# Optimization experiments

Measured on AMD Instinct MI355X. Metric: run time of the kernel, lower is better.

## Reference

```python
import jax, jax.numpy as jnp
import numpy as np

NUM_HEADS = 8
MASK_NEG = -1e30


def setup_inputs() -> dict:
    key = jax.random.key(0)
    k1, k2, k3 = jax.random.split(key, 3)
    B, S, D = 8, 2048, 128
    queries = jax.random.normal(k1, (B, S, D), dtype=jnp.float32)
    mask = jnp.ones((B, S), dtype=jnp.float32)
    # kernel_size=1 Conv1D with no bias == dense matmul over last dim
    W_q = jax.random.normal(k2, (D, D), dtype=jnp.float32) * (D ** -0.5)
    W_mem = jax.random.normal(k3, (D, 2 * D), dtype=jnp.float32) * (D ** -0.5)
    return {"queries": queries, "mask": mask, "W_q": W_q, "W_mem": W_mem}


def _split_heads(x, h):
    # [B, S, D] -> [B, h, S, D/h]
    B, S, D = x.shape
    return x.reshape(B, S, h, D // h).transpose(0, 2, 1, 3)


def reference(queries, mask, W_q, W_mem):
    B, S, D = queries.shape
    h = NUM_HEADS
    scale = (D // h) ** -0.5
    memory = jnp.einsum('bsd,de->bse', queries, W_mem)   # [B,S,2D]
    query = jnp.einsum('bsd,de->bse', queries, W_q)      # [B,S,D]
    K, V = jnp.split(memory, 2, axis=2)
    Q = _split_heads(query, h) * scale                   # [B,h,S,dh]
    K = _split_heads(K, h)
    V = _split_heads(V, h)
    logits = jnp.einsum('bhqd,bhkd->bhqk', Q, K)         # [B,h,S,S]
    m = mask.reshape(B, 1, 1, S)
    logits = logits + (1.0 - m) * MASK_NEG
    weights = jax.nn.softmax(logits, axis=-1)
    # dropout is identity at inference (training=None)
    x = jnp.einsum('bhqk,bhkd->bhqd', weights, V)        # [B,h,S,dh]
    return x.transpose(0, 2, 1, 3).reshape(B, S, D)
```

## Files before the change

### kernel.cpp

```cpp
#include <hip/hip_runtime.h>
#include <hip/hip_bf16.h>
#include <stdint.h>

#define B_    8
#define S_    2048
#define D_    128
#define H_    8
#define DH_   16
#define BH_   64
#define E_    384
#define NT_   (S_ / 32)

typedef __attribute__((ext_vector_type(4)))  short short4v;
typedef __attribute__((ext_vector_type(8)))  short short8;
typedef __attribute__((ext_vector_type(4)))  float f32x4;
typedef __attribute__((ext_vector_type(16))) float f32x16;

__device__ inline unsigned short f2b(float f) {
    union { __bf16 h; unsigned short u; } t;
    t.h = (__bf16)f;
    return t.u;
}
__device__ inline float b2f(unsigned short u) {
    union { unsigned u; float f; } x; x.u = ((unsigned)u) << 16; return x.f;
}
__device__ inline int dperm(int d) {
    return (d & 3) | ((d & 8) >> 1) | ((d & 4) << 1);
}

__device__ inline void gload_lds16(const void* g, void* l) {
    __builtin_amdgcn_global_load_lds(
        (const __attribute__((address_space(1))) unsigned int*)g,
        (__attribute__((address_space(3))) unsigned int*)l, 16, 0, 0);
}

#define EXPB 16250.7346f

__global__ void wtrans_kernel(const float* __restrict__ Wq,
                              const float* __restrict__ Wmem,
                              unsigned short* __restrict__ wt) {
    int e = blockIdx.x, k = threadIdx.x;
    float v = (e < 128) ? Wq[k * 128 + e] : Wmem[k * 256 + (e - 128)];
    wt[e * 128 + k] = f2b(v);
}

__global__ __launch_bounds__(512) void proj_kernel(
        const float* __restrict__ X, const float* __restrict__ mask,
        const unsigned short* __restrict__ wt,
        unsigned short* __restrict__ Qb, unsigned short* __restrict__ KVf) {
    __shared__ unsigned short Xs[64][136];
    __shared__ unsigned short Vs[64][136];
    __shared__ __align__(16) unsigned short Qls[64][136];
    __shared__ __align__(16) unsigned short Kls[8][2][64][8];
    __shared__ float Ms[64];
    const int tid = threadIdx.x;
    const int b = blockIdx.x & 7, st = blockIdx.x >> 3;
    const int s0 = st * 64;
    const float* Xp = X + ((size_t)b * S_ + s0) * D_;

    for (int i = tid; i < 64 * D_ / 4; i += 512) {
        f32x4 v = __builtin_nontemporal_load((const f32x4*)Xp + i);
        int row = i >> 5, c4 = (i & 31) * 4;
        Xs[row][c4 + 0] = f2b(v[0]); Xs[row][c4 + 1] = f2b(v[1]);
        Xs[row][c4 + 2] = f2b(v[2]); Xs[row][c4 + 3] = f2b(v[3]);
    }
    if (tid < 64) Ms[tid] = mask[(size_t)b * S_ + s0 + tid];
    __syncthreads();

    const int wid = tid >> 6, lane = tid & 63;
    const int lr = lane & 15, lg = lane >> 4;
    const float qscale = 0.25f * 1.44269504088896f;

    for (int ci = 0; ci < 3; ++ci) {
        const int ct = wid + ci * 8;
        const int e0 = ct * 16;
        short4v bfr[8];
        #pragma unroll
        for (int kk = 0; kk < 8; ++kk)
            bfr[kk] = *(const short4v*)&wt[(e0 + lr) * 128 + kk * 16 + lg * 4];
        for (int rt = 0; rt < 4; ++rt) {
            f32x4 acc; acc[0] = acc[1] = acc[2] = acc[3] = 0.f;
            #pragma unroll
            for (int kk = 0; kk < 8; ++kk) {
                short4v a = *(const short4v*)&Xs[rt * 16 + lr][kk * 16 + lg * 4];
                acc = __builtin_amdgcn_mfma_f32_16x16x16bf16_1k(a, bfr[kk], acc, 0, 0, 0);
            }
            const int e = e0 + lr;
            #pragma unroll
            for (int r = 0; r < 4; ++r) {
                const int sl = rt * 16 + lg * 4 + r;
                const float v = acc[r];
                if (e < 128) {
                    int hh = e >> 4, d = dperm(e & 15);
                    Qls[sl][hh * 16 + d] = f2b(v * qscale);
                } else if (e < 256) {
                    int ek = e - 128, hh = ek >> 4, d = dperm(ek & 15);
                    int t = sl >> 5, qq = sl & 31;
                    int l = qq + 32 * (d >> 3), jj = d & 7;
                    Kls[hh][t][l][jj] = f2b(v);
                } else {
                    Vs[sl][e - 256] = f2b(v);
                }
            }
        }
    }
    __syncthreads();

    for (int c = tid; c < 1024; c += 512) {
        const int hh = c >> 7, sl = (c >> 1) & 63, half = c & 1;
        *(short8*)&Qb[(((size_t)b * H_ + hh) * S_ + s0 + sl) * DH_ + half * 8] =
            *(const short8*)&Qls[sl][hh * 16 + half * 8];
    }
    for (int c = tid; c < 1024; c += 512) {
        const int hh = c >> 7, t = (c >> 6) & 1, lc = c & 63;
        *(short8*)&KVf[((size_t)(b * H_ + hh) * NT_ + st * 2 + t) * 1536 + lc * 8] =
            *(const short8*)&Kls[hh][t][lc][0];
    }

    for (int j = tid; j < H_ * 2 * 2 * 64; j += 512) {
        const int l = j & 63, f = (j >> 6) & 1, t = (j >> 7) & 1, hh = j >> 8;
        const int q = l & 31, h = l >> 5;
        const int vrow = (q < 16) ? q : 16;
        const int T = st * 2 + t;
        unsigned short* dst =
            KVf + ((size_t)(b * H_ + hh) * NT_ + T) * 1536 + (1 + f) * 512 + l * 8;
        union { unsigned short us[8]; short8 v; } o;
        #pragma unroll
        for (int e = 0; e < 8; ++e) {
            const int p = f * 16 + 8 * h + e;
            const int sl = (p & 16) | dperm(p & 15);
            const int srow = t * 32 + sl;
            const float mk = Ms[srow];
            o.us[e] = f2b((vrow == 16) ? mk : b2f(Vs[srow][hh * 16 + vrow]) * mk);
        }
        *(short8*)dst = o.v;
    }
}

__global__ __launch_bounds__(512, 4) void attn_kernel(
        const unsigned short* __restrict__ Qb, const unsigned short* __restrict__ KVf,
        float* __restrict__ out) {
    const int tid = threadIdx.x;
    const int wid = tid >> 6, lane = tid & 63;
    const int q = lane & 31, h = lane >> 5;
    const int p = blockIdx.x;
    const int bh = (p & 7) * 8 + ((p >> 3) & 7);
    const int qs = p >> 6;
    const int q0 = qs * 256 + wid * 32;

    __shared__ unsigned short buf[2][8][3][64][8];

    const unsigned short* kv = KVf + (size_t)bh * NT_ * 1536 + (size_t)lane * 8;

    const short8 qf = *(const short8*)&Qb[((size_t)bh * S_ + q0 + q) * DH_ + 8 * h];

    f32x16 accA, accB, z;
    #pragma unroll
    for (int i = 0; i < 16; ++i) { accA[i] = 0.f; accB[i] = 0.f; z[i] = 0.f; }

    f32x16 sA, sB;
    short8 pA0, pA1, pB0, pB1;

#define STAGE(C_)                                                              \
    {                                                                          \
        const int tt_ = (C_) * 4 + (wid & 3) + ((wid >> 2) * 32);              \
        const unsigned short* g_ = kv + (size_t)tt_ * 1536;                    \
        unsigned short* d_ = &buf[(C_) & 1][wid][0][0][0];                     \
        gload_lds16(g_,        d_);                                            \
        gload_lds16(g_ + 512,  d_ + 512);                                      \
        gload_lds16(g_ + 1024, d_ + 1024);                                     \
    }

#define FENCE_BAR()                                                            \
    asm volatile("s_waitcnt lgkmcnt(0) vmcnt(0)" ::: "memory");                \
    __builtin_amdgcn_sched_barrier(0);                                         \
    __builtin_amdgcn_s_barrier();                                              \
    __builtin_amdgcn_sched_barrier(0);

#define EXP_PV(ACC_, S_, V0_, V1_)                                             \
    {                                                                          \
        union { unsigned u[4]; short8 v; } b0, b1;                             \
        _Pragma("unroll")                                                      \
        for (int i = 0; i < 4; ++i) {                                          \
            const int l0 = (int)__builtin_fmaf(S_[2 * i],     128.f, EXPB);    \
            const int h0 = (int)__builtin_fmaf(S_[2 * i + 1], 128.f, EXPB);    \
            b0.u[i] = (unsigned)l0 | ((unsigned)h0 << 16);                     \
            const int l1 = (int)__builtin_fmaf(S_[8 + 2 * i],     128.f, EXPB);\
            const int h1 = (int)__builtin_fmaf(S_[8 + 2 * i + 1], 128.f, EXPB);\
            b1.u[i] = (unsigned)l1 | ((unsigned)h1 << 16);                     \
        }                                                                      \
        ACC_ = __builtin_amdgcn_mfma_f32_32x32x16_bf16(V0_, b0.v, ACC_, 0, 0, 0); \
        ACC_ = __builtin_amdgcn_mfma_f32_32x32x16_bf16(V1_, b1.v, ACC_, 0, 0, 0); \
    }

#define PAIR_STEP(BI_, I_)                                                     \
    {                                                                          \
        const short8 kfA = *(const short8*)&buf[BI_][I_][0][lane][0];          \
        const short8 nA0 = *(const short8*)&buf[BI_][I_][1][lane][0];          \
        const short8 nA1 = *(const short8*)&buf[BI_][I_][2][lane][0];          \
        const short8 kfB = *(const short8*)&buf[BI_][4 + I_][0][lane][0];      \
        const short8 nB0 = *(const short8*)&buf[BI_][4 + I_][1][lane][0];      \
        const short8 nB1 = *(const short8*)&buf[BI_][4 + I_][2][lane][0];      \
        EXP_PV(accA, sA, pA0, pA1);                                            \
        EXP_PV(accB, sB, pB0, pB1);                                            \
        sA = __builtin_amdgcn_mfma_f32_32x32x16_bf16(kfA, qf, z, 0, 0, 0);     \
        sB = __builtin_amdgcn_mfma_f32_32x32x16_bf16(kfB, qf, z, 0, 0, 0);     \
        pA0 = nA0; pA1 = nA1; pB0 = nB0; pB1 = nB1;                            \
    }

#define PRIME(BI_, I_)                                                         \
    {                                                                          \
        const short8 kfA = *(const short8*)&buf[BI_][I_][0][lane][0];          \
        pA0 = *(const short8*)&buf[BI_][I_][1][lane][0];                       \
        pA1 = *(const short8*)&buf[BI_][I_][2][lane][0];                       \
        const short8 kfB = *(const short8*)&buf[BI_][4 + I_][0][lane][0];      \
        pB0 = *(const short8*)&buf[BI_][4 + I_][1][lane][0];                   \
        pB1 = *(const short8*)&buf[BI_][4 + I_][2][lane][0];                   \
        sA = __builtin_amdgcn_mfma_f32_32x32x16_bf16(kfA, qf, z, 0, 0, 0);     \
        sB = __builtin_amdgcn_mfma_f32_32x32x16_bf16(kfB, qf, z, 0, 0, 0);     \
    }

    STAGE(0);
    FENCE_BAR();
    STAGE(1);
    PRIME(0, 0);

    for (int c = 0; c < 8; ++c) {
        if (c > 0) {
            FENCE_BAR();
            if (c < 7) STAGE(c + 1);
        }
        #pragma unroll
        for (int i = 0; i < 4; ++i) {
            if (c == 0 && i == 0) continue;
            PAIR_STEP(c & 1, i);
        }
    }
    EXP_PV(accA, sA, pA0, pA1);
    EXP_PV(accB, sB, pB0, pB1);
#undef STAGE
#undef FENCE_BAR
#undef EXP_PV
#undef PAIR_STEP
#undef PRIME

    const int b = bh >> 3, head = bh & 7;
    float* obase = out + ((size_t)b * S_ + q0 + q) * D_ + head * DH_ + 4 * h;
    float o[16];
    #pragma unroll
    for (int i = 0; i < 16; ++i) o[i] = accA[i] + accB[i];
    const float r = 1.0f / o[8];
    *(float4*)obase       = make_float4(o[0] * r, o[1] * r, o[2] * r, o[3] * r);
    *(float4*)(obase + 8) = make_float4(o[4] * r, o[5] * r, o[6] * r, o[7] * r);
}

extern "C" void kernel_launch(void* const* d_in, const int* in_sizes, int n_in,
                              void* d_out, int out_size, void* d_ws, size_t ws_size,
                              hipStream_t stream) {
    const float* X    = (const float*)d_in[0];
    const float* mask = (const float*)d_in[1];
    const float* Wq   = (const float*)d_in[2];
    const float* Wmem = (const float*)d_in[3];
    float* out = (float*)d_out;

    unsigned short* Qb  = (unsigned short*)d_ws;
    unsigned short* KVf = Qb + (size_t)BH_ * S_ * DH_;
    unsigned short* wt  = KVf + (size_t)BH_ * NT_ * 1536;

    wtrans_kernel<<<E_, 128, 0, stream>>>(Wq, Wmem, wt);
    proj_kernel<<<B_ * S_ / 64, 512, 0, stream>>>(X, mask, wt, Qb, KVf);
    attn_kernel<<<BH_ * 8, 512, 0, stream>>>(Qb, KVf, out);
}
```

Before: 53.45 us.

## Shrink attention blocks to four waves and triple-buffer KV staging with partial waits

The attention kernel now launches 256-thread blocks covering 128 queries each, doubling the grid to 1024 blocks. KV tiles are staged through a three-slot LDS ring, and the barrier waits with vmcnt(3), so one prefetch stays in flight while the current tile is consumed. This is meant to hide global-to-LDS latency better and to improve occupancy and load balance across CUs. The cost is twice as many blocks re-reading the same KV data, which raises L2 traffic, plus a fully unrolled schedule that is longer to compile and harder to verify.

```diff
diff --git a/kernel.cpp b/kernel.cpp
--- a/kernel.cpp
+++ b/kernel.cpp
@@ -137,7 +137,7 @@
     }
 }
 
-__global__ __launch_bounds__(512, 4) void attn_kernel(
+__global__ __launch_bounds__(256, 4) void attn_kernel(
         const unsigned short* __restrict__ Qb, const unsigned short* __restrict__ KVf,
         float* __restrict__ out) {
     const int tid = threadIdx.x;
@@ -145,10 +145,10 @@
     const int q = lane & 31, h = lane >> 5;
     const int p = blockIdx.x;
     const int bh = (p & 7) * 8 + ((p >> 3) & 7);
-    const int qs = p >> 6;
-    const int q0 = qs * 256 + wid * 32;
-
-    __shared__ unsigned short buf[2][8][3][64][8];
+    const int qt = p >> 6;
+    const int q0 = qt * 128 + wid * 32;
+
+    __shared__ unsigned short buf[3][4][3][64][8];
 
     const unsigned short* kv = KVf + (size_t)bh * NT_ * 1536 + (size_t)lane * 8;
 
@@ -163,15 +163,21 @@
 
 #define STAGE(C_)                                                              \
     {                                                                          \
-        const int tt_ = (C_) * 4 + (wid & 3) + ((wid >> 2) * 32);              \
+        const int tt_ = (C_) * 2 + (wid & 1) + 32 * (wid >> 1);                \
         const unsigned short* g_ = kv + (size_t)tt_ * 1536;                    \
-        unsigned short* d_ = &buf[(C_) & 1][wid][0][0][0];                     \
+        unsigned short* d_ = &buf[(C_) % 3][wid][0][0][0];                     \
         gload_lds16(g_,        d_);                                            \
         gload_lds16(g_ + 512,  d_ + 512);                                      \
         gload_lds16(g_ + 1024, d_ + 1024);                                     \
     }
 
-#define FENCE_BAR()                                                            \
+#define FENCE_CNT()                                                            \
+    asm volatile("s_waitcnt lgkmcnt(0) vmcnt(3)" ::: "memory");                \
+    __builtin_amdgcn_sched_barrier(0);                                         \
+    __builtin_amdgcn_s_barrier();                                              \
+    __builtin_amdgcn_sched_barrier(0);
+
+#define FENCE_ALL()                                                            \
     asm volatile("s_waitcnt lgkmcnt(0) vmcnt(0)" ::: "memory");                \
     __builtin_amdgcn_sched_barrier(0);                                         \
     __builtin_amdgcn_s_barrier();                                              \
@@ -198,9 +204,9 @@
         const short8 kfA = *(const short8*)&buf[BI_][I_][0][lane][0];          \
         const short8 nA0 = *(const short8*)&buf[BI_][I_][1][lane][0];          \
         const short8 nA1 = *(const short8*)&buf[BI_][I_][2][lane][0];          \
-        const short8 kfB = *(const short8*)&buf[BI_][4 + I_][0][lane][0];      \
-        const short8 nB0 = *(const short8*)&buf[BI_][4 + I_][1][lane][0];      \
-        const short8 nB1 = *(const short8*)&buf[BI_][4 + I_][2][lane][0];      \
+        const short8 kfB = *(const short8*)&buf[BI_][2 + I_][0][lane][0];      \
+        const short8 nB0 = *(const short8*)&buf[BI_][2 + I_][1][lane][0];      \
+        const short8 nB1 = *(const short8*)&buf[BI_][2 + I_][2][lane][0];      \
         EXP_PV(accA, sA, pA0, pA1);                                            \
         EXP_PV(accB, sB, pB0, pB1);                                            \
         sA = __builtin_amdgcn_mfma_f32_32x32x16_bf16(kfA, qf, z, 0, 0, 0);     \
@@ -208,38 +214,40 @@
         pA0 = nA0; pA1 = nA1; pB0 = nB0; pB1 = nB1;                            \
     }
 
-#define PRIME(BI_, I_)                                                         \
-    {                                                                          \
-        const short8 kfA = *(const short8*)&buf[BI_][I_][0][lane][0];          \
-        pA0 = *(const short8*)&buf[BI_][I_][1][lane][0];                       \
-        pA1 = *(const short8*)&buf[BI_][I_][2][lane][0];                       \
-        const short8 kfB = *(const short8*)&buf[BI_][4 + I_][0][lane][0];      \
-        pB0 = *(const short8*)&buf[BI_][4 + I_][1][lane][0];                   \
-        pB1 = *(const short8*)&buf[BI_][4 + I_][2][lane][0];                   \
+#define PRIME()                                                                \
+    {                                                                          \
+        const short8 kfA = *(const short8*)&buf[0][0][0][lane][0];             \
+        pA0 = *(const short8*)&buf[0][0][1][lane][0];                          \
+        pA1 = *(const short8*)&buf[0][0][2][lane][0];                          \
+        const short8 kfB = *(const short8*)&buf[0][2][0][lane][0];             \
+        pB0 = *(const short8*)&buf[0][2][1][lane][0];                          \
+        pB1 = *(const short8*)&buf[0][2][2][lane][0];                          \
         sA = __builtin_amdgcn_mfma_f32_32x32x16_bf16(kfA, qf, z, 0, 0, 0);     \
         sB = __builtin_amdgcn_mfma_f32_32x32x16_bf16(kfB, qf, z, 0, 0, 0);     \
     }
 
-    STAGE(0);
-    FENCE_BAR();
-    STAGE(1);
-    PRIME(0, 0);
-
-    for (int c = 0; c < 8; ++c) {
-        if (c > 0) {
-            FENCE_BAR();
-            if (c < 7) STAGE(c + 1);
-        }
-        #pragma unroll
-        for (int i = 0; i < 4; ++i) {
-            if (c == 0 && i == 0) continue;
-            PAIR_STEP(c & 1, i);
-        }
-    }
+    STAGE(0); STAGE(1);
+    FENCE_CNT();
+    STAGE(2);
+    PRIME();
+    PAIR_STEP(0, 1);
+
+    #pragma unroll
+    for (int c = 1; c <= 14; ++c) {
+        FENCE_CNT();
+        if (c <= 13) STAGE(c + 2);
+        PAIR_STEP(c % 3, 0);
+        PAIR_STEP(c % 3, 1);
+    }
+
+    FENCE_ALL();
+    PAIR_STEP(0, 0);
+    PAIR_STEP(0, 1);
     EXP_PV(accA, sA, pA0, pA1);
     EXP_PV(accB, sB, pB0, pB1);
 #undef STAGE
-#undef FENCE_BAR
+#undef FENCE_CNT
+#undef FENCE_ALL
 #undef EXP_PV
 #undef PAIR_STEP
 #undef PRIME
@@ -269,5 +277,5 @@
 
     wtrans_kernel<<<E_, 128, 0, stream>>>(Wq, Wmem, wt);
     proj_kernel<<<B_ * S_ / 64, 512, 0, stream>>>(X, mask, wt, Qb, KVf);
-    attn_kernel<<<BH_ * 8, 512, 0, stream>>>(Qb, KVf, out);
-}
+    attn_kernel<<<BH_ * (S_ / 128), 256, 0, stream>>>(Qb, KVf, out);
+}
```

Result: slower. 61.54 us (+15.1%).
